# Kernel tuning notes

Measured on AMD Instinct MI355X. Metric: run time of the kernel, lower is better.

## Reference

```python
import jax, jax.numpy as jnp
import numpy as np

N, E = 10000, 160000
IN_DIM, HID, EDGE_DIM = 512, 256, 51
EPS = 1e-8


def setup_inputs() -> dict:
    key = jax.random.key(0)
    ks = jax.random.split(key, 16)
    s = 0.02
    return {
        'h': jax.random.normal(ks[0], (N, IN_DIM), jnp.float32),
        'edge_index': jax.random.randint(ks[1], (2, E), 0, N, jnp.int64 if jax.config.jax_enable_x64 else jnp.int32),
        'edge_attr': jax.random.normal(ks[2], (E, EDGE_DIM), jnp.float32),
        'pos': jax.random.normal(ks[3], (N, 3), jnp.float32),
        # edge_mlp: Linear(2*IN_DIM+EDGE_DIM+1 -> HID), SiLU, Linear(HID -> HID), SiLU
        'eW1': jax.random.normal(ks[4], (2 * IN_DIM + EDGE_DIM + 1, HID), jnp.float32) * s,
        'eb1': jnp.zeros((HID,), jnp.float32),
        'eW2': jax.random.normal(ks[5], (HID, HID), jnp.float32) * s,
        'eb2': jnp.zeros((HID,), jnp.float32),
        # coord_mlp: Linear(HID->HID), SiLU, Linear(HID->1, no bias, tiny init)
        'cW1': jax.random.normal(ks[6], (HID, HID), jnp.float32) * s,
        'cb1': jnp.zeros((HID,), jnp.float32),
        'cW2': jax.random.normal(ks[7], (HID, 1), jnp.float32) * 0.001,
        # node_mlp: Linear(IN_DIM+HID -> HID), SiLU, Linear(HID -> HID)
        'nW1': jax.random.normal(ks[8], (IN_DIM + HID, HID), jnp.float32) * s,
        'nb1': jnp.zeros((HID,), jnp.float32),
        'nW2': jax.random.normal(ks[9], (HID, HID), jnp.float32) * s,
        'nb2': jnp.zeros((HID,), jnp.float32),
    }


def reference(h, edge_index, edge_attr, pos, eW1, eb1, eW2, eb2, cW1, cb1, cW2, nW1, nb1, nW2, nb2):
    row, col = edge_index[0], edge_index[1]
    diff = pos[row] - pos[col]                                   # [E,3]
    radial = jnp.sqrt(jnp.sum(diff * diff, axis=-1, keepdims=True)) + EPS  # [E,1]
    edge_in = jnp.concatenate([h[row], h[col], edge_attr, radial], axis=-1)  # [E,1076]
    e = jax.nn.silu(edge_in @ eW1 + eb1)
    e = jax.nn.silu(e @ eW2 + eb2)                               # [E,HID]
    coord_update = jax.nn.silu(e @ cW1 + cb1) @ cW2              # [E,1]
    coord_update = jnp.clip(coord_update, -1.0, 1.0)
    trans = coord_update * diff                                  # [E,3]
    agg_coord = jax.ops.segment_sum(trans, row, num_segments=pos.shape[0])
    pos_new = pos + agg_coord
    agg_node = jax.ops.segment_sum(e, row, num_segments=h.shape[0])  # [N,HID]
    h_new = jax.nn.silu(jnp.concatenate([h, agg_node], axis=-1) @ nW1 + nb1) @ nW2 + nb2
    # residual skipped: h_new last dim (HID=256) != h last dim (IN_DIM=512)
    return (h_new, pos_new)
```

## Files before the change

### kernel.cpp

```cpp
#include <hip/hip_runtime.h>
#include <hip/hip_bf16.h>

#define N_NODES 10000
#define N_PAD   10016
#define E_EDGES 160000
#define EB 32
#define NTILES (E_EDGES / EB)
#define HID 256

typedef __attribute__((ext_vector_type(4))) float f32x4;
typedef __attribute__((ext_vector_type(8))) short bf16x8;
typedef __attribute__((ext_vector_type(8))) unsigned short u16x8;
typedef __attribute__((ext_vector_type(4))) unsigned u32x4;
typedef unsigned short u16;
typedef __attribute__((address_space(1))) const unsigned int gu32;
typedef __attribute__((address_space(3))) unsigned int lu32;

__device__ __forceinline__ float silu_f(float x) { return x / (1.0f + __expf(-x)); }

__device__ __forceinline__ u16 f2bf(float f) {
    unsigned x = __float_as_uint(f);
    unsigned r = x + 0x7FFFu + ((x >> 16) & 1u);
    return (u16)(r >> 16);
}
__device__ __forceinline__ float bf2f(u16 u) {
    return __uint_as_float(((unsigned)u) << 16);
}
__device__ __forceinline__ unsigned cvtpk(float a, float b) {
    unsigned r;
    asm("v_cvt_pk_bf16_f32 %0, %1, %2" : "=v"(r) : "v"(a), "v"(b));
    return r;
}
__device__ __forceinline__ f32x4 mfma16(bf16x8 a, bf16x8 b, f32x4 c) {
    return __builtin_amdgcn_mfma_f32_16x16x32_bf16(a, b, c, 0, 0, 0);
}
__device__ __forceinline__ int actb(int row, int elem) {
    return (row * 512 + elem * 2) ^ ((row & 7) << 4);
}
__device__ __forceinline__ int xcd_swz(int bid, int nwg) {
    int qq = nwg >> 3, r8 = nwg & 7;
    int xcd = bid & 7, sub = bid >> 3;
    return (xcd < r8 ? xcd * (qq + 1) : r8 * (qq + 1) + (xcd - r8) * qq) + sub;
}

__global__ __launch_bounds__(256) void prep_weights(
    const float* __restrict__ eW1, const float* __restrict__ eW2,
    const float* __restrict__ cW1, const float* __restrict__ nW1,
    const float* __restrict__ nW2,
    u16* __restrict__ Wt3, u16* __restrict__ e1pt,
    u16* __restrict__ n1t, u16* __restrict__ n2t,
    u16* __restrict__ e2s, u16* __restrict__ c1s)
{
    const int y = blockIdx.y;
    if (y >= 6) {
        if (blockIdx.x >= 32) return;
        const float* W = (y == 6) ? eW2 : cW1;
        u16* dst = (y == 6) ? e2s : c1s;
        int T = blockIdx.x * 256 + threadIdx.x;
        int kc = T >> 10, rem = T & 1023;
        int q = rem >> 6, lane = rem & 63;
        int n = (q >> 2) * 64 + (q & 3) * 16 + (lane & 15);
        int kbase = kc * 32 + (lane >> 4) * 8;
        u16x8 o;
#pragma unroll
        for (int jj = 0; jj < 8; ++jj)
            o[jj] = f2bf(W[(size_t)(kbase + jj) * 256 + n]);
        *(u16x8*)&dst[(size_t)T * 8] = o;
        return;
    }
    const float* src; u16* dstp; int Ks, Kd;
    switch (y) {
        case 0: src = eW1;                dstp = Wt3;                Ks = 512; Kd = 512; break;
        case 1: src = eW1 + 512 * 256;    dstp = Wt3 + 256 * 512;    Ks = 512; Kd = 512; break;
        case 2: src = nW1;                dstp = Wt3 + 2 * 256 * 512; Ks = 512; Kd = 512; break;
        case 3: src = eW1 + 1024 * 256;   dstp = e1pt;               Ks = 52;  Kd = 64;  break;
        case 4: src = nW1 + 512 * 256;    dstp = n1t;                Ks = 256; Kd = 256; break;
        default: src = nW2;               dstp = n2t;                Ks = 256; Kd = 256; break;
    }
    int idx = blockIdx.x * 256 + threadIdx.x;
    if (idx < 256 * Kd) {
        int n = idx / Kd, k = idx - n * Kd;
        dstp[idx] = (k < Ks) ? f2bf(src[(size_t)k * 256 + n]) : (u16)0;
    }
}

__global__ __launch_bounds__(256) void conv_h(const float* __restrict__ h, u16* __restrict__ hb)
{
    size_t base = ((size_t)blockIdx.x * 256 + threadIdx.x) * 8;
    int row = (int)(base >> 9);
    u16x8 o;
    if (row < N_NODES) {
        const float4 f0 = *(const float4*)&h[base];
        const float4 f1 = *(const float4*)&h[base + 4];
        o[0] = f2bf(f0.x); o[1] = f2bf(f0.y); o[2] = f2bf(f0.z); o[3] = f2bf(f0.w);
        o[4] = f2bf(f1.x); o[5] = f2bf(f1.y); o[6] = f2bf(f1.z); o[7] = f2bf(f1.w);
    } else {
        o = (u16x8)0;
    }
    *(u16x8*)&hb[base] = o;
}

__global__ __launch_bounds__(256) void hist_kernel(const int* __restrict__ row,
                                                   int* __restrict__ hist)
{
    int e = blockIdx.x * 256 + threadIdx.x;
    if (e < E_EDGES) atomicAdd(&hist[row[e]], 1);
}

#define SCAN_PER 40
__global__ __launch_bounds__(256) void scan_kernel(const int* __restrict__ hist,
                                                   int* __restrict__ rowptr)
{
    __shared__ int a[256];
    const int t = threadIdx.x;
    const int base = t * SCAN_PER;
    int s = 0;
    for (int i = 0; i < SCAN_PER; ++i) {
        int b = base + i;
        if (b < N_PAD) s += hist[b];
    }
    a[t] = s;
    __syncthreads();
    for (int off = 1; off < 256; off <<= 1) {
        int v = (t >= off) ? a[t - off] : 0;
        __syncthreads();
        a[t] += v;
        __syncthreads();
    }
    int run = a[t] - s;
    for (int i = 0; i < SCAN_PER; ++i) {
        int b = base + i;
        if (b < N_PAD) { rowptr[b] = run; run += hist[b]; }
    }
    if (t == 255) rowptr[N_PAD] = a[255];
}

__global__ __launch_bounds__(256) void scatter_kernel(const int* __restrict__ row,
                                                      const int* __restrict__ rowptr,
                                                      int* __restrict__ cnt,
                                                      int* __restrict__ eorder)
{
    int e = blockIdx.x * 256 + threadIdx.x;
    if (e < E_EDGES) {
        int r = row[e];
        int p = rowptr[r] + atomicAdd(&cnt[r], 1);
        eorder[p] = e;
    }
}

__global__ __launch_bounds__(256) void precompute_X(
    const u16* __restrict__ hb, const u16* __restrict__ Wt3, u16* __restrict__ Xb)
{
    const int n0b = blockIdx.x * 32;
    const int which = blockIdx.y;
    const int j = threadIdx.x, wv = j >> 6, lane = j & 63;
    const int ml = lane & 15, g = lane >> 4;
    const int n0 = wv * 64;
    const u16* W = Wt3 + (size_t)which * 256 * 512;

    f32x4 acc[2][4];
    const f32x4 z = {0.f, 0.f, 0.f, 0.f};
#pragma unroll
    for (int mt = 0; mt < 2; ++mt)
#pragma unroll
        for (int nt = 0; nt < 4; ++nt) acc[mt][nt] = z;

    for (int kc = 0; kc < 16; ++kc) {
        bf16x8 a0 = *(const bf16x8*)&hb[(size_t)(n0b + ml) * 512 + kc * 32 + g * 8];
        bf16x8 a1 = *(const bf16x8*)&hb[(size_t)(n0b + 16 + ml) * 512 + kc * 32 + g * 8];
#pragma unroll
        for (int nt = 0; nt < 4; ++nt) {
            bf16x8 b = *(const bf16x8*)&W[(size_t)(n0 + nt * 16 + ml) * 512 + kc * 32 + g * 8];
            acc[0][nt] = mfma16(a0, b, acc[0][nt]);
            acc[1][nt] = mfma16(a1, b, acc[1][nt]);
        }
    }
#pragma unroll
    for (int mt = 0; mt < 2; ++mt)
#pragma unroll
        for (int nt = 0; nt < 4; ++nt) {
            int col = n0 + nt * 16 + ml;
#pragma unroll
            for (int i = 0; i < 4; ++i) {
                int row = n0b + mt * 16 + g * 4 + i;
                Xb[(size_t)row * 768 + which * 256 + col] = f2bf(acc[mt][nt][i]);
            }
        }
}

__global__ __launch_bounds__(256) void edge_kernel(
    const u16* __restrict__ Xb, const float* __restrict__ pos,
    const int* __restrict__ eidx, const float* __restrict__ eattr,
    const int* __restrict__ eorder,
    const u16* __restrict__ e1pt, const float* __restrict__ eb1,
    const u16* __restrict__ e2s, const float* __restrict__ eb2,
    const u16* __restrict__ c1s, const float* __restrict__ cb1,
    const float* __restrict__ cW2,
    float* __restrict__ agg_node, float* __restrict__ agg_coord)
{
    __shared__ u16 attr[EB * 64];
    __shared__ u16 bufA[EB * 256];
    __shared__ u16 ldsB[2][4096];
    __shared__ int ri_s[EB], ci_s[EB], es_s[EB];
    __shared__ float rad_s[EB], dif_s[EB][3];
    __shared__ float red[EB * 4];

    const int j = threadIdx.x, w = j >> 6, lane = j & 63;
    const int ml = lane & 15, g = lane >> 4;
    const int n0 = w * 64;
    const f32x4 z = {0.f, 0.f, 0.f, 0.f};

    const int wg = xcd_swz(blockIdx.x, gridDim.x);
    const int e0 = wg * EB;

#pragma unroll
    for (int i = 0; i < 2; ++i) {
        const u16* src = e2s + (size_t)((4 * w + i) * 512 + lane * 8);
        u16* dst = &ldsB[0][w * 1024 + i * 512 + lane * 8];
        __builtin_amdgcn_global_load_lds((gu32*)src, (lu32*)dst, 16, 0, 0);
    }

    if (j < EB) {
        int e = eorder[e0 + j];
        es_s[j] = e;
        int r = eidx[e], c = eidx[E_EDGES + e];
        ri_s[j] = r; ci_s[j] = c;
        float dx = pos[r * 3 + 0] - pos[c * 3 + 0];
        float dy = pos[r * 3 + 1] - pos[c * 3 + 1];
        float dz = pos[r * 3 + 2] - pos[c * 3 + 2];
        dif_s[j][0] = dx; dif_s[j][1] = dy; dif_s[j][2] = dz;
        rad_s[j] = sqrtf(dx * dx + dy * dy + dz * dz) + 1e-8f;
    }
    asm volatile("s_waitcnt lgkmcnt(0)" ::: "memory");
    __builtin_amdgcn_s_barrier();

#pragma unroll
    for (int t = 0; t < 4; ++t) {
        int li = t * 256 + j;
        int e = li >> 5, c = li & 31;
        const u16x8 xr = *(const u16x8*)&Xb[(size_t)ri_s[e] * 768 + c * 8];
        const u16x8 xc = *(const u16x8*)&Xb[(size_t)ci_s[e] * 768 + 256 + c * 8];
        u32x4 o;
#pragma unroll
        for (int k = 0; k < 4; ++k)
            o[k] = cvtpk(bf2f(xr[2 * k]) + bf2f(xc[2 * k]),
                         bf2f(xr[2 * k + 1]) + bf2f(xc[2 * k + 1]));
        *(u32x4*)((char*)bufA + ((e * 512 + c * 16) ^ ((e & 7) << 4))) = o;
    }
    for (int li = j; li < EB * 64; li += 256) {
        int row = li >> 6, k = li & 63;
        float v = (k < 51) ? eattr[(size_t)es_s[row] * 51 + k] : (k == 51 ? rad_s[row] : 0.f);
        int byte = (row * 128 + k * 2) ^ ((row & 7) << 4);
        attr[byte >> 1] = f2bf(v);
    }
    asm volatile("s_waitcnt lgkmcnt(0)" ::: "memory");
    __builtin_amdgcn_s_barrier();

    f32x4 acc[2][4];

#pragma unroll
    for (int mt = 0; mt < 2; ++mt)
#pragma unroll
        for (int nt = 0; nt < 4; ++nt) acc[mt][nt] = z;
#pragma unroll
    for (int kc = 0; kc < 2; ++kc) {
        bf16x8 a0 = *(const bf16x8*)((const char*)attr + ((ml * 128 + (kc * 32 + g * 8) * 2) ^ ((ml & 7) << 4)));
        bf16x8 a1 = *(const bf16x8*)((const char*)attr + (((16 + ml) * 128 + (kc * 32 + g * 8) * 2) ^ ((ml & 7) << 4)));
#pragma unroll
        for (int nt = 0; nt < 4; ++nt) {
            bf16x8 b = *(const bf16x8*)&e1pt[(size_t)(n0 + nt * 16 + ml) * 64 + kc * 32 + g * 8];
            acc[0][nt] = mfma16(a0, b, acc[0][nt]);
            acc[1][nt] = mfma16(a1, b, acc[1][nt]);
        }
    }
#pragma unroll
    for (int nt = 0; nt < 4; ++nt) {
        int col = n0 + nt * 16 + ml;
        float b1 = eb1[col];
#pragma unroll
        for (int mt = 0; mt < 2; ++mt)
#pragma unroll
            for (int i = 0; i < 4; ++i) {
                int row = mt * 16 + g * 4 + i;
                int off = actb(row, col) >> 1;
                float v = acc[mt][nt][i] + b1 + bf2f(bufA[off]);
                bufA[off] = f2bf(silu_f(v));
            }
    }
    asm volatile("s_waitcnt lgkmcnt(0)" ::: "memory");
    __builtin_amdgcn_s_barrier();

#pragma unroll
    for (int mt = 0; mt < 2; ++mt)
#pragma unroll
        for (int nt = 0; nt < 4; ++nt) acc[mt][nt] = z;
    for (int hc = 0; hc < 16; ++hc) {
        int kc = hc >> 1, h = hc & 1;
        if (hc < 15) {
            int kc1 = (hc + 1) >> 1, h1 = (hc + 1) & 1;
#pragma unroll
            for (int i = 0; i < 2; ++i) {
                const u16* src = e2s + (size_t)kc1 * 8192 + (4 * w + 2 * h1 + i) * 512 + lane * 8;
                u16* dst = &ldsB[(hc + 1) & 1][w * 1024 + i * 512 + lane * 8];
                __builtin_amdgcn_global_load_lds((gu32*)src, (lu32*)dst, 16, 0, 0);
            }
            asm volatile("s_waitcnt vmcnt(2)" ::: "memory");
        } else {
            asm volatile("s_waitcnt vmcnt(0)" ::: "memory");
        }
        __builtin_amdgcn_sched_barrier(0);
        bf16x8 a0 = *(const bf16x8*)((const char*)bufA + actb(ml, kc * 32 + g * 8));
        bf16x8 a1 = *(const bf16x8*)((const char*)bufA + actb(16 + ml, kc * 32 + g * 8));
#pragma unroll
        for (int i = 0; i < 2; ++i) {
            int nt = 2 * h + i;
            bf16x8 b = *(const bf16x8*)&ldsB[hc & 1][w * 1024 + i * 512 + lane * 8];
            acc[0][nt] = mfma16(a0, b, acc[0][nt]);
            acc[1][nt] = mfma16(a1, b, acc[1][nt]);
        }
    }
    asm volatile("s_waitcnt lgkmcnt(0)" ::: "memory");
    __builtin_amdgcn_s_barrier();

#pragma unroll
    for (int i = 0; i < 2; ++i) {
        const u16* src = c1s + (size_t)((4 * w + i) * 512 + lane * 8);
        u16* dst = &ldsB[0][w * 1024 + i * 512 + lane * 8];
        __builtin_amdgcn_global_load_lds((gu32*)src, (lu32*)dst, 16, 0, 0);
    }

#pragma unroll
    for (int nt = 0; nt < 4; ++nt) {
        int col = n0 + nt * 16 + ml;
        float b2 = eb2[col];
#pragma unroll
        for (int mt = 0; mt < 2; ++mt)
#pragma unroll
            for (int i = 0; i < 4; ++i) {
                int row = mt * 16 + g * 4 + i;
                bufA[actb(row, col) >> 1] = f2bf(silu_f(acc[mt][nt][i] + b2));
            }
    }
    asm volatile("s_waitcnt lgkmcnt(0)" ::: "memory");
    __builtin_amdgcn_s_barrier();

#pragma unroll
    for (int mt = 0; mt < 2; ++mt)
#pragma unroll
        for (int nt = 0; nt < 4; ++nt) acc[mt][nt] = z;
    for (int hc = 0; hc < 16; ++hc) {
        int kc = hc >> 1, h = hc & 1;
        if (hc < 15) {
            int kc1 = (hc + 1) >> 1, h1 = (hc + 1) & 1;
#pragma unroll
            for (int i = 0; i < 2; ++i) {
                const u16* src = c1s + (size_t)kc1 * 8192 + (4 * w + 2 * h1 + i) * 512 + lane * 8;
                u16* dst = &ldsB[(hc + 1) & 1][w * 1024 + i * 512 + lane * 8];
                __builtin_amdgcn_global_load_lds((gu32*)src, (lu32*)dst, 16, 0, 0);
            }
            asm volatile("s_waitcnt vmcnt(2)" ::: "memory");
        } else {
            asm volatile("s_waitcnt vmcnt(0)" ::: "memory");
        }
        __builtin_amdgcn_sched_barrier(0);
        bf16x8 a0 = *(const bf16x8*)((const char*)bufA + actb(ml, kc * 32 + g * 8));
        bf16x8 a1 = *(const bf16x8*)((const char*)bufA + actb(16 + ml, kc * 32 + g * 8));
#pragma unroll
        for (int i = 0; i < 2; ++i) {
            int nt = 2 * h + i;
            bf16x8 b = *(const bf16x8*)&ldsB[hc & 1][w * 1024 + i * 512 + lane * 8];
            acc[0][nt] = mfma16(a0, b, acc[0][nt]);
            acc[1][nt] = mfma16(a1, b, acc[1][nt]);
        }
    }

    {
        int cur = ri_s[0];
        float s = bf2f(bufA[actb(0, j) >> 1]);
#pragma unroll
        for (int m = 1; m < EB; ++m) {
            int r = ri_s[m];
            float v = bf2f(bufA[actb(m, j) >> 1]);
            if (r != cur) {
                atomicAdd(&agg_node[(size_t)cur * 256 + j], s);
                s = 0.f; cur = r;
            }
            s += v;
        }
        atomicAdd(&agg_node[(size_t)cur * 256 + j], s);
    }

    float p[2][4] = {{0.f, 0.f, 0.f, 0.f}, {0.f, 0.f, 0.f, 0.f}};
#pragma unroll
    for (int nt = 0; nt < 4; ++nt) {
        int col = n0 + nt * 16 + ml;
        float b3 = cb1[col];
        float w2 = cW2[col];
#pragma unroll
        for (int mt = 0; mt < 2; ++mt)
#pragma unroll
            for (int i = 0; i < 4; ++i)
                p[mt][i] += silu_f(acc[mt][nt][i] + b3) * w2;
    }
#pragma unroll
    for (int mt = 0; mt < 2; ++mt)
#pragma unroll
        for (int i = 0; i < 4; ++i) {
            float v = p[mt][i];
            v += __shfl_xor(v, 1);
            v += __shfl_xor(v, 2);
            v += __shfl_xor(v, 4);
            v += __shfl_xor(v, 8);
            p[mt][i] = v;
        }
    if (ml == 0) {
#pragma unroll
        for (int mt = 0; mt < 2; ++mt)
#pragma unroll
            for (int i = 0; i < 4; ++i)
                red[(mt * 16 + g * 4 + i) * 4 + w] = p[mt][i];
    }
    __syncthreads();
    if (j < EB) {
        float u = red[j * 4 + 0] + red[j * 4 + 1] + red[j * 4 + 2] + red[j * 4 + 3];
        u = fminf(fmaxf(u, -1.f), 1.f);
        int rr = ri_s[j];
        atomicAdd(&agg_coord[(size_t)rr * 3 + 0], u * dif_s[j][0]);
        atomicAdd(&agg_coord[(size_t)rr * 3 + 1], u * dif_s[j][1]);
        atomicAdd(&agg_coord[(size_t)rr * 3 + 2], u * dif_s[j][2]);
    }
}

__global__ __launch_bounds__(256) void node_kernel(
    const u16* __restrict__ Xb, const float* __restrict__ agg_node,
    const float* __restrict__ agg_coord, const float* __restrict__ pos,
    const u16* __restrict__ n1t, const float* __restrict__ nb1,
    const u16* __restrict__ n2t, const float* __restrict__ nb2,
    float* __restrict__ out)
{
    __shared__ u16 act1[32 * 256];
    __shared__ u16 act2[32 * 256];
    const int n0b = blockIdx.x * 32;
    const int j = threadIdx.x, wv = j >> 6, lane = j & 63;
    const int ml = lane & 15, g = lane >> 4;
    const int n0 = wv * 64;
    const f32x4 z = {0.f, 0.f, 0.f, 0.f};

    for (int li = j; li < 32 * 256; li += 256) {
        int r = li >> 8, c = li & 255;
        act1[actb(r, c) >> 1] = f2bf(agg_node[(size_t)(n0b + r) * 256 + c]);
    }
    __syncthreads();

    f32x4 acc[2][4];
#pragma unroll
    for (int mt = 0; mt < 2; ++mt)
#pragma unroll
        for (int nt = 0; nt < 4; ++nt) acc[mt][nt] = z;
    for (int kc = 0; kc < 8; ++kc) {
        bf16x8 a0 = *(const bf16x8*)((const char*)act1 + actb(ml, kc * 32 + g * 8));
        bf16x8 a1 = *(const bf16x8*)((const char*)act1 + actb(16 + ml, kc * 32 + g * 8));
#pragma unroll
        for (int nt = 0; nt < 4; ++nt) {
            bf16x8 b = *(const bf16x8*)&n1t[(size_t)(n0 + nt * 16 + ml) * 256 + kc * 32 + g * 8];
            acc[0][nt] = mfma16(a0, b, acc[0][nt]);
            acc[1][nt] = mfma16(a1, b, acc[1][nt]);
        }
    }
#pragma unroll
    for (int mt = 0; mt < 2; ++mt)
#pragma unroll
        for (int nt = 0; nt < 4; ++nt) {
            int col = n0 + nt * 16 + ml;
            float b1 = nb1[col];
#pragma unroll
            for (int i = 0; i < 4; ++i) {
                int m = mt * 16 + g * 4 + i;
                float v = acc[mt][nt][i] + b1 + bf2f(Xb[(size_t)(n0b + m) * 768 + 512 + col]);
                act2[actb(m, col) >> 1] = f2bf(silu_f(v));
            }
        }
    __syncthreads();
#pragma unroll
    for (int mt = 0; mt < 2; ++mt)
#pragma unroll
        for (int nt = 0; nt < 4; ++nt) acc[mt][nt] = z;
    for (int kc = 0; kc < 8; ++kc) {
        bf16x8 a0 = *(const bf16x8*)((const char*)act2 + actb(ml, kc * 32 + g * 8));
        bf16x8 a1 = *(const bf16x8*)((const char*)act2 + actb(16 + ml, kc * 32 + g * 8));
#pragma unroll
        for (int nt = 0; nt < 4; ++nt) {
            bf16x8 b = *(const bf16x8*)&n2t[(size_t)(n0 + nt * 16 + ml) * 256 + kc * 32 + g * 8];
            acc[0][nt] = mfma16(a0, b, acc[0][nt]);
            acc[1][nt] = mfma16(a1, b, acc[1][nt]);
        }
    }
#pragma unroll
    for (int mt = 0; mt < 2; ++mt)
#pragma unroll
        for (int nt = 0; nt < 4; ++nt) {
            int col = n0 + nt * 16 + ml;
            float b2 = nb2[col];
#pragma unroll
            for (int i = 0; i < 4; ++i) {
                int row = n0b + mt * 16 + g * 4 + i;
                if (row < N_NODES)
                    out[(size_t)row * 256 + col] = acc[mt][nt][i] + b2;
            }
        }
    if (j < 96) {
        int idx = n0b * 3 + j;
        if (idx < N_NODES * 3)
            out[(size_t)N_NODES * 256 + idx] = pos[idx] + agg_coord[idx];
    }
}

extern "C" void kernel_launch(void* const* d_in, const int* in_sizes, int n_in,
                              void* d_out, int out_size, void* d_ws, size_t ws_size,
                              hipStream_t stream)
{
    (void)in_sizes; (void)n_in; (void)out_size; (void)ws_size;
    const float* h     = (const float*)d_in[0];
    const int*   eidx  = (const int*)d_in[1];
    const float* eattr = (const float*)d_in[2];
    const float* pos   = (const float*)d_in[3];
    const float* eW1   = (const float*)d_in[4];
    const float* eb1   = (const float*)d_in[5];
    const float* eW2   = (const float*)d_in[6];
    const float* eb2   = (const float*)d_in[7];
    const float* cW1   = (const float*)d_in[8];
    const float* cb1   = (const float*)d_in[9];
    const float* cW2   = (const float*)d_in[10];
    const float* nW1   = (const float*)d_in[11];
    const float* nb1   = (const float*)d_in[12];
    const float* nW2   = (const float*)d_in[13];
    const float* nb2   = (const float*)d_in[14];
    float* out = (float*)d_out;

    u16* Xb   = (u16*)d_ws;
    u16* hb   = Xb + (size_t)N_PAD * 768;
    u16* Wt3  = hb + (size_t)N_PAD * 512;
    u16* e1pt = Wt3 + 3 * 256 * 512;
    u16* n1t  = e1pt + 256 * 64;
    u16* n2t  = n1t + 256 * 256;
    u16* e2s  = n2t + 256 * 256;
    u16* c1s  = e2s + 65536;
    float* agg_node  = (float*)(c1s + 65536);
    float* agg_coord = agg_node + (size_t)N_PAD * 256;
    int* hist   = (int*)(agg_coord + (size_t)N_PAD * 3);
    int* cnt    = hist + N_PAD;
    int* rowptr = cnt + N_PAD;
    int* eorder = rowptr + N_PAD + 1;

    hipMemsetAsync(agg_node, 0, (size_t)N_PAD * 259 * sizeof(float), stream);
    hipMemsetAsync(hist, 0, (size_t)2 * N_PAD * sizeof(int), stream);

    prep_weights<<<dim3(512, 8), 256, 0, stream>>>(eW1, eW2, cW1, nW1, nW2,
                                                   Wt3, e1pt, n1t, n2t, e2s, c1s);
    conv_h<<<(N_PAD * 512 / 8) / 256, 256, 0, stream>>>(h, hb);

    hist_kernel<<<(E_EDGES + 255) / 256, 256, 0, stream>>>(eidx, hist);
    scan_kernel<<<1, 256, 0, stream>>>(hist, rowptr);
    scatter_kernel<<<(E_EDGES + 255) / 256, 256, 0, stream>>>(eidx, rowptr, cnt, eorder);

    precompute_X<<<dim3(N_PAD / 32, 3), 256, 0, stream>>>(hb, Wt3, Xb);

    edge_kernel<<<NTILES, 256, 0, stream>>>(
        Xb, pos, eidx, eattr, eorder, e1pt, eb1, e2s, eb2, c1s, cb1, cW2,
        agg_node, agg_coord);

    node_kernel<<<N_PAD / 32, 256, 0, stream>>>(
        Xb, agg_node, agg_coord, pos, n1t, nb1, n2t, nb2, out);
}
```

Baseline: 340.1 us.

## Split edge kernel into first-layer and second-layer kernels staged through workspace

Result: faster. 313.4 us (-7.8%).

```diff
diff --git a/kernel.cpp b/kernel.cpp
--- a/kernel.cpp
+++ b/kernel.cpp
@@ -188,22 +188,18 @@
         }
 }
 
-__global__ __launch_bounds__(256) void edge_kernel(
+__global__ __launch_bounds__(256) void e1_kernel(
     const u16* __restrict__ Xb, const float* __restrict__ pos,
     const int* __restrict__ eidx, const float* __restrict__ eattr,
     const int* __restrict__ eorder,
     const u16* __restrict__ e1pt, const float* __restrict__ eb1,
-    const u16* __restrict__ e2s, const float* __restrict__ eb2,
-    const u16* __restrict__ c1s, const float* __restrict__ cb1,
-    const float* __restrict__ cW2,
-    float* __restrict__ agg_node, float* __restrict__ agg_coord)
+    int t0, u16* __restrict__ act1s,
+    int* __restrict__ ri_sorted, float* __restrict__ difp)
 {
     __shared__ u16 attr[EB * 64];
     __shared__ u16 bufA[EB * 256];
-    __shared__ u16 ldsB[2][4096];
     __shared__ int ri_s[EB], ci_s[EB], es_s[EB];
-    __shared__ float rad_s[EB], dif_s[EB][3];
-    __shared__ float red[EB * 4];
+    __shared__ float rad_s[EB];
 
     const int j = threadIdx.x, w = j >> 6, lane = j & 63;
     const int ml = lane & 15, g = lane >> 4;
@@ -211,28 +207,23 @@
     const f32x4 z = {0.f, 0.f, 0.f, 0.f};
 
     const int wg = xcd_swz(blockIdx.x, gridDim.x);
-    const int e0 = wg * EB;
-
-#pragma unroll
-    for (int i = 0; i < 2; ++i) {
-        const u16* src = e2s + (size_t)((4 * w + i) * 512 + lane * 8);
-        u16* dst = &ldsB[0][w * 1024 + i * 512 + lane * 8];
-        __builtin_amdgcn_global_load_lds((gu32*)src, (lu32*)dst, 16, 0, 0);
-    }
+    const int e0 = (t0 + wg) * EB;
 
     if (j < EB) {
         int e = eorder[e0 + j];
         es_s[j] = e;
         int r = eidx[e], c = eidx[E_EDGES + e];
         ri_s[j] = r; ci_s[j] = c;
+        ri_sorted[e0 + j] = r;
         float dx = pos[r * 3 + 0] - pos[c * 3 + 0];
         float dy = pos[r * 3 + 1] - pos[c * 3 + 1];
         float dz = pos[r * 3 + 2] - pos[c * 3 + 2];
-        dif_s[j][0] = dx; dif_s[j][1] = dy; dif_s[j][2] = dz;
+        difp[e0 + j] = dx;
+        difp[E_EDGES + e0 + j] = dy;
+        difp[2 * E_EDGES + e0 + j] = dz;
         rad_s[j] = sqrtf(dx * dx + dy * dy + dz * dz) + 1e-8f;
     }
-    asm volatile("s_waitcnt lgkmcnt(0)" ::: "memory");
-    __builtin_amdgcn_s_barrier();
+    __syncthreads();
 
 #pragma unroll
     for (int t = 0; t < 4; ++t) {
@@ -253,11 +244,9 @@
         int byte = (row * 128 + k * 2) ^ ((row & 7) << 4);
         attr[byte >> 1] = f2bf(v);
     }
-    asm volatile("s_waitcnt lgkmcnt(0)" ::: "memory");
-    __builtin_amdgcn_s_barrier();
+    __syncthreads();
 
     f32x4 acc[2][4];
-
 #pragma unroll
     for (int mt = 0; mt < 2; ++mt)
 #pragma unroll
@@ -287,8 +276,57 @@
                 bufA[off] = f2bf(silu_f(v));
             }
     }
-    asm volatile("s_waitcnt lgkmcnt(0)" ::: "memory");
+    __syncthreads();
+
+    const size_t obase = (size_t)wg * (EB * 256);
+#pragma unroll
+    for (int i = 0; i < 4; ++i) {
+        int li = i * 256 + j;
+        *(u16x8*)&act1s[obase + (size_t)li * 8] = *(const u16x8*)&bufA[li * 8];
+    }
+}
+
+__global__ __launch_bounds__(256) void e2_kernel(
+    const u16* __restrict__ act1s,
+    const u16* __restrict__ e2s, const float* __restrict__ eb2,
+    const u16* __restrict__ c1s, const float* __restrict__ cb1,
+    const float* __restrict__ cW2,
+    const int* __restrict__ ri_sorted, const float* __restrict__ difp,
+    int t0, float* __restrict__ agg_node, float* __restrict__ agg_coord)
+{
+    __shared__ u16 bufA[EB * 256];
+    __shared__ u16 ldsB[2][4096];
+    __shared__ int ri_s[EB];
+    __shared__ float red[EB * 4];
+
+    const int j = threadIdx.x, w = j >> 6, lane = j & 63;
+    const int ml = lane & 15, g = lane >> 4;
+    const int n0 = w * 64;
+    const f32x4 z = {0.f, 0.f, 0.f, 0.f};
+
+    const int wg = xcd_swz(blockIdx.x, gridDim.x);
+    const int e0 = (t0 + wg) * EB;
+
+    {
+        const size_t gbase = (size_t)wg * (EB * 256);
+#pragma unroll
+        for (int i = 0; i < 4; ++i) {
+            const u16* src = act1s + gbase + (size_t)(i * 256 + j) * 8;
+            u16* dst = &bufA[(i * 256 + j) * 8];
+            __builtin_amdgcn_global_load_lds((gu32*)src, (lu32*)dst, 16, 0, 0);
+        }
+#pragma unroll
+        for (int i = 0; i < 2; ++i) {
+            const u16* src = e2s + (size_t)((4 * w + i) * 512 + lane * 8);
+            u16* dst = &ldsB[0][w * 1024 + i * 512 + lane * 8];
+            __builtin_amdgcn_global_load_lds((gu32*)src, (lu32*)dst, 16, 0, 0);
+        }
+    }
+    if (j < EB) ri_s[j] = ri_sorted[e0 + j];
+    asm volatile("s_waitcnt vmcnt(2) lgkmcnt(0)" ::: "memory");
     __builtin_amdgcn_s_barrier();
+
+    f32x4 acc[2][4];
 
 #pragma unroll
     for (int mt = 0; mt < 2; ++mt)
@@ -372,22 +410,6 @@
             acc[0][nt] = mfma16(a0, b, acc[0][nt]);
             acc[1][nt] = mfma16(a1, b, acc[1][nt]);
         }
-    }
-
-    {
-        int cur = ri_s[0];
-        float s = bf2f(bufA[actb(0, j) >> 1]);
-#pragma unroll
-        for (int m = 1; m < EB; ++m) {
-            int r = ri_s[m];
-            float v = bf2f(bufA[actb(m, j) >> 1]);
-            if (r != cur) {
-                atomicAdd(&agg_node[(size_t)cur * 256 + j], s);
-                s = 0.f; cur = r;
-            }
-            s += v;
-        }
-        atomicAdd(&agg_node[(size_t)cur * 256 + j], s);
     }
 
     float p[2][4] = {{0.f, 0.f, 0.f, 0.f}, {0.f, 0.f, 0.f, 0.f}};
@@ -425,9 +447,28 @@
         float u = red[j * 4 + 0] + red[j * 4 + 1] + red[j * 4 + 2] + red[j * 4 + 3];
         u = fminf(fmaxf(u, -1.f), 1.f);
         int rr = ri_s[j];
-        atomicAdd(&agg_coord[(size_t)rr * 3 + 0], u * dif_s[j][0]);
-        atomicAdd(&agg_coord[(size_t)rr * 3 + 1], u * dif_s[j][1]);
-        atomicAdd(&agg_coord[(size_t)rr * 3 + 2], u * dif_s[j][2]);
+        atomicAdd(&agg_coord[(size_t)rr * 3 + 0], u * difp[e0 + j]);
+        atomicAdd(&agg_coord[(size_t)rr * 3 + 1], u * difp[E_EDGES + e0 + j]);
+        atomicAdd(&agg_coord[(size_t)rr * 3 + 2], u * difp[2 * E_EDGES + e0 + j]);
+    }
+
+    {
+        float vreg[EB];
+#pragma unroll
+        for (int m = 0; m < EB; ++m)
+            vreg[m] = bf2f(bufA[actb(m, j) >> 1]);
+        int cur = ri_s[0];
+        float s = vreg[0];
+#pragma unroll
+        for (int m = 1; m < EB; ++m) {
+            int r = ri_s[m];
+            if (r != cur) {
+                atomicAdd(&agg_node[(size_t)cur * 256 + j], s);
+                s = 0.f; cur = r;
+            }
+            s += vreg[m];
+        }
+        atomicAdd(&agg_node[(size_t)cur * 256 + j], s);
     }
 }
 
@@ -519,7 +560,7 @@
                               void* d_out, int out_size, void* d_ws, size_t ws_size,
                               hipStream_t stream)
 {
-    (void)in_sizes; (void)n_in; (void)out_size; (void)ws_size;
+    (void)in_sizes; (void)n_in; (void)out_size;
     const float* h     = (const float*)d_in[0];
     const int*   eidx  = (const int*)d_in[1];
     const float* eattr = (const float*)d_in[2];
@@ -551,6 +592,15 @@
     int* cnt    = hist + N_PAD;
     int* rowptr = cnt + N_PAD;
     int* eorder = rowptr + N_PAD + 1;
+    int* ri_sorted = eorder + E_EDGES;
+    float* difp = (float*)(ri_sorted + E_EDGES);
+    char* wend = (char*)(difp + (size_t)3 * E_EDGES);
+    u16* act1s = (u16*)(((uintptr_t)wend + 255) & ~(uintptr_t)255);
+
+    size_t avail = ws_size - (size_t)((char*)act1s - (char*)d_ws);
+    int tiles_cap = (int)(avail / (EB * 256 * sizeof(u16)));
+    int chunk = tiles_cap < NTILES ? tiles_cap : NTILES;
+    if (chunk < 1) chunk = 1;
 
     hipMemsetAsync(agg_node, 0, (size_t)N_PAD * 259 * sizeof(float), stream);
     hipMemsetAsync(hist, 0, (size_t)2 * N_PAD * sizeof(int), stream);
@@ -565,9 +615,13 @@
 
     precompute_X<<<dim3(N_PAD / 32, 3), 256, 0, stream>>>(hb, Wt3, Xb);
 
-    edge_kernel<<<NTILES, 256, 0, stream>>>(
-        Xb, pos, eidx, eattr, eorder, e1pt, eb1, e2s, eb2, c1s, cb1, cW2,
-        agg_node, agg_coord);
+    for (int c = 0; c < NTILES; c += chunk) {
+        int g = (NTILES - c) < chunk ? (NTILES - c) : chunk;
+        e1_kernel<<<g, 256, 0, stream>>>(Xb, pos, eidx, eattr, eorder,
+                                         e1pt, eb1, c, act1s, ri_sorted, difp);
+        e2_kernel<<<g, 256, 0, stream>>>(act1s, e2s, eb2, c1s, cb1, cW2,
+                                         ri_sorted, difp, c, agg_node, agg_coord);
+    }
 
     node_kernel<<<N_PAD / 32, 256, 0, stream>>>(
         Xb, agg_node, agg_coord, pos, n1t, nb1, n2t, nb2, out);
```
